# Kernel optimization log

Measured on AMD Instinct MI355X. Metric: run time of the kernel, lower is better.

Reference implementation:

```python
import jax, jax.numpy as jnp
import numpy as np

N_IN, N_LAT, LEN_T, N_SHIFT = 128, 21, 51, 50
N_HID, BATCH = 4, 2048


def identity_init(n_rows, n_cols):
    A = np.zeros((n_rows, n_cols), np.float32)
    if n_rows >= n_cols:
        k = n_rows - n_cols + 1
        for c in range(n_cols):
            A[c:c + k, c] = 1.0 / k
    else:
        k = n_cols - n_rows + 1
        for r in range(n_rows):
            A[r, r:r + k] = 1.0 / k
    return jnp.asarray(A)


def setup_inputs() -> dict:
    key = jax.random.key(0)
    ks = jax.random.split(key, 8)
    s = 0.05
    return {
        'inputs': jax.random.normal(ks[0], (BATCH, LEN_T, N_IN), dtype=jnp.float32),
        'enc_W': jax.random.normal(ks[1], (N_HID, N_IN, N_IN), dtype=jnp.float32) * s,
        'enc_b': jnp.zeros((N_HID, N_IN), jnp.float32),
        'enc_Wout': jax.random.normal(ks[2], (N_IN, N_IN), dtype=jnp.float32) * s,
        'enc_bout': jnp.zeros((N_IN,), jnp.float32),
        'dec_W': jax.random.normal(ks[3], (N_HID, N_IN, N_IN), dtype=jnp.float32) * s,
        'dec_b': jnp.zeros((N_HID, N_IN), jnp.float32),
        'dec_Wout': jax.random.normal(ks[4], (N_IN, N_IN), dtype=jnp.float32) * s,
        'dec_bout': jnp.zeros((N_IN,), jnp.float32),
        'W_enc_inner': identity_init(N_IN, N_LAT),
        'L': jnp.eye(N_LAT, dtype=jnp.float32),
        'W_dec_inner': identity_init(N_LAT, N_IN),
    }


def res_block(x, Ws, bs, Wout, bout):
    # DenseResBlock: ReLU hidden dense stack + linear output + identity skip
    h = x
    for i in range(Ws.shape[0]):
        h = jax.nn.relu(h @ Ws[i] + bs[i])
    return h @ Wout + bout + x


def reference(inputs, enc_W, enc_b, enc_Wout, enc_bout,
              dec_W, dec_b, dec_Wout, dec_bout,
              W_enc_inner, L, W_dec_inner):
    B = inputs.shape[0]
    len_pred = LEN_T - N_SHIFT  # = 1

    # ---- autoencoder branch (all timesteps flattened into rows) ----
    auto_in = inputs.reshape(-1, N_IN)                       # [B*T, n_in]
    part_enc = res_block(auto_in, enc_W, enc_b, enc_Wout, enc_bout)
    full_enc = part_enc @ W_enc_inner                        # [B*T, n_lat]
    part_dec = full_enc @ W_dec_inner                        # [B*T, n_in]
    autoencoder_output = res_block(part_dec, dec_W, dec_b, dec_Wout, dec_bout)
    autoencoder_output = autoencoder_output.reshape(B, LEN_T, N_IN)
    outer_auto_output = res_block(part_enc, dec_W, dec_b, dec_Wout, dec_bout)
    outer_auto_output = outer_auto_output.reshape(B, LEN_T, N_IN)

    # ---- prediction branch: recurrent application of Koopman operator L ----
    pred_in = inputs[:, :len_pred, :].reshape(-1, N_IN)      # [B*len_pred, n_in]
    cur = res_block(pred_in, enc_W, enc_b, enc_Wout, enc_bout) @ W_enc_inner

    def step(cur_enc, _):
        adv = cur_enc @ L                                    # [B*len_pred, n_lat]
        dec = res_block(adv @ W_dec_inner, dec_W, dec_b, dec_Wout, dec_bout)
        return adv, dec

    _, preds = jax.lax.scan(step, cur, None, length=N_SHIFT)  # [S, B*lp, n_in]
    preds = preds.reshape(N_SHIFT, B, len_pred, N_IN)
    predictions = preds.transpose(1, 0, 2, 3).reshape(B, N_SHIFT * len_pred, N_IN)

    return autoencoder_output, outer_auto_output, predictions
```

## Files before the change

### kernel.cpp

```cpp
#include <hip/hip_runtime.h>
#include <stdint.h>


typedef _Float16 h8 __attribute__((ext_vector_type(8)));
typedef _Float16 h4 __attribute__((ext_vector_type(4)));
typedef float    f4 __attribute__((ext_vector_type(4)));

#define ROWS_AUTO 104448
#define NT64      1632
#define NUNITS    2432

#define WT_ENCW      0
#define WT_ENCWOUT   (4*16384)
#define WT_DECW      (5*16384)
#define WT_DECWOUT   (9*16384)
#define WT_COMB      (10*16384)

#define MFULL_OFF_B 0x60000
#define ACH_OFF_B   0x200000
#define PE_OFF_B    0x220000
#define PET0_OFF_B  0x1C00000
#define CTRL_OFF_B  0x1D00000

#define H0 0
#define H1 16384
#define H2 32768
#define H3 49152
#define LDSE (49152 + 2560 + 16)
#define LDSD (65536 + 2560 + 16)

#define hsw(rl, c) ((rl)*256 + ((((c)) ^ ((rl) & 7)) << 4))

#define PIN(B) asm volatile("" : "+v"(B[0]), "+v"(B[1]), "+v"(B[2]), "+v"(B[3]), \
                                 "+v"(B[4]), "+v"(B[5]), "+v"(B[6]), "+v"(B[7]))

__device__ __forceinline__ f4 mfma16(h8 a, h8 b, f4 c) {
  return __builtin_amdgcn_mfma_f32_16x16x32_f16(a, b, c, 0, 0, 0);
}
__device__ __forceinline__ h8 cvt8(f4 a, f4 b) {
  h8 r;
  r[0]=(_Float16)a[0]; r[1]=(_Float16)a[1]; r[2]=(_Float16)a[2]; r[3]=(_Float16)a[3];
  r[4]=(_Float16)b[0]; r[5]=(_Float16)b[1]; r[6]=(_Float16)b[2]; r[7]=(_Float16)b[3];
  return r;
}
__device__ __forceinline__ void loadW(h8 B[8], const _Float16* gW, int nbase, int r15, int hi) {
#pragma unroll
  for (int nt = 0; nt < 2; ++nt)
#pragma unroll
    for (int ks = 0; ks < 4; ++ks)
      B[nt*4+ks] = *(const h8*)(gW + (size_t)(nbase + nt*16 + r15)*128 + ks*32 + hi*8);
}

__device__ __forceinline__ void mmF4s(const char* sm, int hb, const h8 B[8],
                                      f4 acc[4][2], int r15, int hi) {
#pragma unroll
  for (int rt = 0; rt < 4; ++rt) { acc[rt][0] = (f4){0,0,0,0}; acc[rt][1] = (f4){0,0,0,0}; }
#pragma unroll
  for (int ks = 0; ks < 4; ++ks) {
    int c = ks*4 + hi;
    h8 a[4];
#pragma unroll
    for (int rt = 0; rt < 4; ++rt) a[rt] = *(const h8*)(sm + hb + hsw(rt*16 + r15, c));
#pragma unroll
    for (int rt = 0; rt < 4; ++rt) {
      acc[rt][0] = mfma16(B[ks],   a[rt], acc[rt][0]);
      acc[rt][1] = mfma16(B[4+ks], a[rt], acc[rt][1]);
    }
  }
}

__device__ __forceinline__ void hw4s(char* sm, int hb, int wbase, const f4 acc[4][2],
                                     const float* bl, int bo, int r15, int hi) {
  f4 bb0 = *(const f4*)(bl + bo + wbase + hi*4);
  f4 bb1 = *(const f4*)(bl + bo + wbase + 16 + hi*4);
  int bo2 = (hi & 1) * 8;
#pragma unroll
  for (int nt = 0; nt < 2; ++nt) {
    int c = ((wbase + nt*16) >> 3) + (hi >> 1);
    f4 bb = nt ? bb1 : bb0;
#pragma unroll
    for (int rt = 0; rt < 4; ++rt) {
      int row = rt*16 + r15;
      h4 p;
#pragma unroll
      for (int d = 0; d < 4; ++d) p[d] = (_Float16)fmaxf(acc[rt][nt][d] + bb[d], 0.f);
      *(h4*)(sm + hb + row*256 + ((c ^ (row & 7)) << 4) + bo2) = p;
    }
  }
}
__device__ __forceinline__ void hw4r(char* sm, int hb, int wbase, const f4 acc[4][2],
                                     int r15, int hi) {
  int bo2 = (hi & 1) * 8;
#pragma unroll
  for (int nt = 0; nt < 2; ++nt) {
    int c = ((wbase + nt*16) >> 3) + (hi >> 1);
#pragma unroll
    for (int rt = 0; rt < 4; ++rt) {
      int row = rt*16 + r15;
      h4 p;
#pragma unroll
      for (int d = 0; d < 4; ++d) p[d] = (_Float16)acc[rt][nt][d];
      *(h4*)(sm + hb + row*256 + ((c ^ (row & 7)) << 4) + bo2) = p;
    }
  }
}

__device__ __forceinline__ void epi_direct(const char* sm, int hskip, int wbase,
                                           const f4 acc[4][2], const float* bl,
                                           float* dst, int rstride, int r15, int hi) {
  f4 bb0 = *(const f4*)(bl + 512 + wbase + hi*4);
  f4 bb1 = *(const f4*)(bl + 512 + wbase + 16 + hi*4);
  int bo2 = (hi & 1) * 8;
#pragma unroll
  for (int nt = 0; nt < 2; ++nt) {
    int c = ((wbase + nt*16) >> 3) + (hi >> 1);
    int n0 = wbase + nt*16 + hi*4;
    f4 bb = nt ? bb1 : bb0;
#pragma unroll
    for (int rt = 0; rt < 4; ++rt) {
      int row = rt*16 + r15;
      h4 sk = *(const h4*)(sm + hskip + row*256 + ((c ^ (row & 7)) << 4) + bo2);
      f4 v;
#pragma unroll
      for (int d = 0; d < 4; ++d) v[d] = acc[rt][nt][d] + bb[d] + (float)sk[d];
      *(f4*)(dst + (size_t)row*rstride + n0) = v;
    }
  }
}

#define LAYD(HIN, HOUT, BW, BO) do {                                 \
    mmF4s(sm, HIN, BW, acc, r15, hi);                                \
    hw4s(sm, HOUT, wbase, acc, bl, BO, r15, hi);                     \
    __syncthreads();                                                 \
  } while (0)

#define TICKET(CTR, LIM, VAR)                                        \
    __syncthreads();                                                 \
    if (tid == 0) *tk = __hip_atomic_fetch_add(&(CTR), 1,            \
                          __ATOMIC_RELAXED, __HIP_MEMORY_SCOPE_AGENT); \
    __syncthreads();                                                 \
    int VAR = *tk;                                                   \
    if (VAR >= (LIM)) break;


__global__ __launch_bounds__(512) void k_prep(
    const float* __restrict__ encW, const float* __restrict__ encWout,
    const float* __restrict__ decW, const float* __restrict__ decWout,
    const float* __restrict__ L,
    _Float16* __restrict__ wt, float* __restrict__ ach) {
  __shared__ float chA[441], chB[441];
  int m = blockIdx.y, tid = threadIdx.x;
  if (m == 10) {
    if (blockIdx.x != 0) return;
    if (tid < 441) chA[tid] = L[tid];
    __syncthreads();
    for (int s = 0; s < 50; ++s) {
      if (tid < 441) ach[s*441 + tid] = chA[tid];
      if (s == 49) break;
      if (tid < 441) {
        int i = tid / 21, j = tid % 21; float a = 0.f;
        for (int k = 0; k < 21; ++k) a += chA[i*21 + k] * L[k*21 + j];
        chB[tid] = a;
      }
      __syncthreads();
      if (tid < 441) chA[tid] = chB[tid];
      __syncthreads();
    }
    return;
  }
  int idx = blockIdx.x*512 + tid;
  if (idx >= 16384) return;
  const float* src; _Float16* dst;
  if (m < 4)       { src = encW + m*16384;     dst = wt + WT_ENCW + m*16384; }
  else if (m == 4) { src = encWout;            dst = wt + WT_ENCWOUT; }
  else if (m < 9)  { src = decW + (m-5)*16384; dst = wt + WT_DECW + (m-5)*16384; }
  else             { src = decWout;            dst = wt + WT_DECWOUT; }
  int n = idx >> 7, k = idx & 127;
  dst[idx] = (_Float16)src[k*128 + n];
}

__global__ __launch_bounds__(512) void k_aux(
    const float* __restrict__ ach, const float* __restrict__ wencI,
    const float* __restrict__ wdecI,
    _Float16* __restrict__ mfull, _Float16* __restrict__ wt) {
  __shared__ float T1[2688];
  __shared__ float sa[441];
  int s = blockIdx.x, t = threadIdx.x;
  if (s < 50) {
    if (t < 441) sa[t] = ach[s*441 + t];
    __syncthreads();
    for (int idx = t; idx < 2688; idx += 512) {
      int k = idx / 21, j = idx % 21;
      float a = 0.f;
      for (int u = 0; u < 21; ++u) a += wencI[k*21 + u] * sa[u*21 + j];
      T1[idx] = a;
    }
  } else {
    for (int idx = t; idx < 2688; idx += 512) T1[idx] = wencI[idx];
  }
  __syncthreads();
  _Float16* dst = (s < 50) ? (mfull + (size_t)s*16384) : (wt + WT_COMB);
  for (int idx = t; idx < 16384; idx += 512) {
    int n = idx >> 7, k = idx & 127;
    float a = 0.f;
    for (int j = 0; j < 21; ++j) a += T1[k*21 + j] * wdecI[j*128 + n];
    dst[idx] = (_Float16)a;
  }
}


__global__ __launch_bounds__(256, 2) void k_enc(
    const float* __restrict__ x, const _Float16* __restrict__ wt,
    const float* __restrict__ enc_b, const float* __restrict__ enc_bout,
    _Float16* __restrict__ pe_ws, _Float16* __restrict__ pet0,
    int* __restrict__ ctrl) {
  __shared__ char sm[LDSE];
  float* bl = (float*)(sm + 49152);
  int* tk = (int*)(sm + 49152 + 2560);
  int tid = threadIdx.x, lane = tid & 63;
  int r15 = lane & 15, hi = lane >> 4;
  int wbase = (tid >> 6) * 32;
  h8 B0[8], B1[8], B2[8], B3[8], B4[8];
  loadW(B0, wt + WT_ENCW,           wbase, r15, hi);
  loadW(B1, wt + WT_ENCW + 16384,   wbase, r15, hi);
  loadW(B2, wt + WT_ENCW + 2*16384, wbase, r15, hi);
  loadW(B3, wt + WT_ENCW + 3*16384, wbase, r15, hi);
  loadW(B4, wt + WT_ENCWOUT,        wbase, r15, hi);
  PIN(B0); PIN(B1); PIN(B2); PIN(B3); PIN(B4);
  bl[tid] = enc_b[tid]; bl[256 + tid] = enc_b[256 + tid];
  if (tid < 128) bl[512 + tid] = enc_bout[tid];
  f4 acc[4][2];

  for (;;) {
    TICKET(ctrl[0], NT64, t);
    size_t rb = (size_t)t * 64;
#pragma unroll
    for (int i = 0; i < 4; ++i) {
      int idx = i*256 + tid, rl = idx >> 4, c = idx & 15;
      const float* s = x + (rb + rl)*128 + c*8;
      f4 v0 = *(const f4*)s, v1 = *(const f4*)(s + 4);
      *(h8*)(sm + H0 + hsw(rl, c)) = cvt8(v0, v1);
    }
    __syncthreads();
    LAYD(H0, H1, B0, 0); LAYD(H1, H2, B1, 128);
    LAYD(H2, H1, B2, 256); LAYD(H1, H2, B3, 384);
    mmF4s(sm, H2, B4, acc, r15, hi);
    {
      f4 bb0 = *(const f4*)(bl + 512 + wbase + hi*4);
      f4 bb1 = *(const f4*)(bl + 512 + wbase + 16 + hi*4);
      int bo2 = (hi & 1) * 8;
#pragma unroll
      for (int nt = 0; nt < 2; ++nt) {
        int c = ((wbase + nt*16) >> 3) + (hi >> 1);
        f4 bb = nt ? bb1 : bb0;
#pragma unroll
        for (int rt = 0; rt < 4; ++rt) {
          int row = rt*16 + r15;
          int soff = H0 + row*256 + ((c ^ (row & 7)) << 4) + bo2;
          h4 sk = *(const h4*)(sm + soff);
          h4 p;
#pragma unroll
          for (int d = 0; d < 4; ++d) p[d] = (_Float16)(acc[rt][nt][d] + bb[d] + (float)sk[d]);
          *(h4*)(sm + soff) = p;
        }
      }
    }
    __syncthreads();
    {
      char* g = (char*)(pe_ws) + (size_t)t*16384;
#pragma unroll
      for (int i = 0; i < 4; ++i) {
        int idx = i*256 + tid, off = idx*16;
        f4 v = *(const f4*)(sm + H0 + off);
        *(f4*)(g + off) = v;
        int rl = idx >> 4, slot = idx & 15;
        size_t rg = rb + (size_t)rl;
        if (rg % 51u == 0u) {
          int c = slot ^ (rl & 7);
          *(f4*)((char*)pet0 + (rg/51u)*256 + c*16) = v;
        }
      }
    }
  }
}


__global__ __launch_bounds__(256, 2) void k_decpred(
    const _Float16* __restrict__ wt, const _Float16* __restrict__ pe_ws,
    const _Float16* __restrict__ pet0, const _Float16* __restrict__ mfull,
    const float* __restrict__ dec_b, const float* __restrict__ dec_bout,
    float* __restrict__ out1, float* __restrict__ out2, float* __restrict__ out3,
    int* __restrict__ ctrl) {
  __shared__ char sm[LDSD];
  float* bl = (float*)(sm + 65536);
  int* tk = (int*)(sm + 65536 + 2560);
  int tid = threadIdx.x, lane = tid & 63;
  int r15 = lane & 15, hi = lane >> 4;
  int wbase = (tid >> 6) * 32;
  h8 B0[8], B1[8], B2[8], B3[8], B4[8];
  loadW(B0, wt + WT_DECW,           wbase, r15, hi);
  loadW(B1, wt + WT_DECW + 16384,   wbase, r15, hi);
  loadW(B2, wt + WT_DECW + 2*16384, wbase, r15, hi);
  loadW(B3, wt + WT_DECW + 3*16384, wbase, r15, hi);
  loadW(B4, wt + WT_DECWOUT,        wbase, r15, hi);
  PIN(B0); PIN(B1); PIN(B2); PIN(B3); PIN(B4);
  bl[tid] = dec_b[tid]; bl[256 + tid] = dec_b[256 + tid];
  if (tid < 128) bl[512 + tid] = dec_bout[tid];
  f4 acc[4][2];

  for (;;) {
    TICKET(ctrl[1], NUNITS, u);
    if (u < NT64) {
      const char* src = (const char*)pe_ws + (size_t)u*16384;
#pragma unroll
      for (int i = 0; i < 4; ++i) {
        int off = (i*256 + tid)*16;
        *(f4*)(sm + H0 + off) = *(const f4*)(src + off);
      }
      __syncthreads();
      LAYD(H0, H1, B0, 0); LAYD(H1, H2, B1, 128);
      LAYD(H2, H1, B2, 256); LAYD(H1, H2, B3, 384);
      mmF4s(sm, H2, B4, acc, r15, hi);
      epi_direct(sm, H0, wbase, acc, bl,
                 out2 + (size_t)u*64*128, 128, r15, hi);
      {
        h8 Bc[8];
        loadW(Bc, wt + WT_COMB, wbase, r15, hi);
        mmF4s(sm, H0, Bc, acc, r15, hi);
      }
      hw4r(sm, H3, wbase, acc, r15, hi);
      __syncthreads();
      LAYD(H3, H0, B0, 0); LAYD(H0, H1, B1, 128);
      LAYD(H1, H0, B2, 256); LAYD(H0, H1, B3, 384);
      mmF4s(sm, H1, B4, acc, r15, hi);
      epi_direct(sm, H3, wbase, acc, bl,
                 out1 + (size_t)u*64*128, 128, r15, hi);
    } else {
      int p = u - NT64, rtile = p / 25, chunk = p % 25;
#pragma unroll
      for (int i = 0; i < 4; ++i) {
        int idx = i*256 + tid, rl = idx >> 4, c = idx & 15;
        f4 v = *(const f4*)((const char*)pet0 + (size_t)(rtile*64 + rl)*256 + c*16);
        *(f4*)(sm + H0 + hsw(rl, c)) = v;
      }
      __syncthreads();
      for (int s = chunk*2; s < chunk*2 + 2; ++s) {
        {
          h8 Bm[8];
          loadW(Bm, mfull + (size_t)s*16384, wbase, r15, hi);
          mmF4s(sm, H0, Bm, acc, r15, hi);
        }
        hw4r(sm, H1, wbase, acc, r15, hi);
        __syncthreads();
        LAYD(H1, H2, B0, 0); LAYD(H2, H3, B1, 128);
        LAYD(H3, H2, B2, 256); LAYD(H2, H3, B3, 384);
        mmF4s(sm, H3, B4, acc, r15, hi);
        epi_direct(sm, H1, wbase, acc, bl,
                   out3 + ((size_t)rtile*64*50 + s)*128, 50*128, r15, hi);
        __syncthreads();
      }
    }
  }
}


extern "C" void kernel_launch(void* const* d_in, const int* in_sizes, int n_in,
                              void* d_out, int out_size, void* d_ws, size_t ws_size,
                              hipStream_t stream) {
  const float* x        = (const float*)d_in[0];
  const float* encW     = (const float*)d_in[1];
  const float* enc_b    = (const float*)d_in[2];
  const float* encWout  = (const float*)d_in[3];
  const float* enc_bout = (const float*)d_in[4];
  const float* decW     = (const float*)d_in[5];
  const float* dec_b    = (const float*)d_in[6];
  const float* decWout  = (const float*)d_in[7];
  const float* dec_bout = (const float*)d_in[8];
  const float* wencI    = (const float*)d_in[9];
  const float* L        = (const float*)d_in[10];
  const float* wdecI    = (const float*)d_in[11];

  char* ws = (char*)d_ws;
  _Float16* wt    = (_Float16*)ws;
  _Float16* mfull = (_Float16*)(ws + MFULL_OFF_B);
  float*    ach   = (float*)(ws + ACH_OFF_B);
  _Float16* pe_ws = (_Float16*)(ws + PE_OFF_B);
  _Float16* pet0  = (_Float16*)(ws + PET0_OFF_B);
  int*      ctrl  = (int*)(ws + CTRL_OFF_B);

  float* out1 = (float*)d_out;
  float* out2 = out1 + (size_t)ROWS_AUTO*128;
  float* out3 = out2 + (size_t)ROWS_AUTO*128;

  hipMemsetAsync(ctrl, 0, sizeof(int)*2, stream);
  hipLaunchKernelGGL(k_prep, dim3(32, 11), dim3(512), 0, stream,
                     encW, encWout, decW, decWout, L, wt, ach);
  hipLaunchKernelGGL(k_aux, dim3(51), dim3(512), 0, stream,
                     ach, wencI, wdecI, mfull, wt);
  hipLaunchKernelGGL(k_enc, dim3(512), dim3(256), 0, stream,
                     x, wt, enc_b, enc_bout, pe_ws, pet0, ctrl);
  hipLaunchKernelGGL(k_decpred, dim3(512), dim3(256), 0, stream,
                     wt, pe_ws, pet0, mfull, dec_b, dec_bout, out1, out2, out3, ctrl);
}
```

Measured before the change: 208.4 us.

## Use 512-thread blocks processing two independent 64-row chains interleaved per barrier

Blocks grow from 256 to 512 threads. Eight waves split each 64-row tile into two 32-row halves, and each block now processes two independent work streams at once: two encoder tiles, the two decoder chains per tile, or two prediction steps. Their layers are interleaved so each barrier covers twice the MFMA work and the two chains overlap. This costs a much larger LDS footprint per block (about 100-117KB) and 512 threads each pinning five weight fragments in registers, which may limit occupancy to one block per CU.

```diff
diff --git a/kernel.cpp b/kernel.cpp
--- a/kernel.cpp
+++ b/kernel.cpp
@@ -8,6 +8,7 @@
 
 #define ROWS_AUTO 104448
 #define NT64      1632
+#define NPAIR     816
 #define NUNITS    2432
 
 #define WT_ENCW      0
@@ -22,12 +23,21 @@
 #define PET0_OFF_B  0x1C00000
 #define CTRL_OFF_B  0x1D00000
 
-#define H0 0
-#define H1 16384
-#define H2 32768
-#define H3 49152
-#define LDSE (49152 + 2560 + 16)
-#define LDSD (65536 + 2560 + 16)
+#define PA 0
+#define PB 16384
+#define UA 32768
+#define VA 49152
+#define UB 65536
+#define VB 81920
+#define LDSE (98304 + 2560 + 16)
+#define PP 0
+#define QQ 16384
+#define UU 32768
+#define VV 49152
+#define XX 65536
+#define YY 81920
+#define ZZ 98304
+#define LDSD (114688 + 2560 + 16)
 
 #define hsw(rl, c) ((rl)*256 + ((((c)) ^ ((rl) & 7)) << 4))
 
@@ -51,26 +61,24 @@
       B[nt*4+ks] = *(const h8*)(gW + (size_t)(nbase + nt*16 + r15)*128 + ks*32 + hi*8);
 }
 
-__device__ __forceinline__ void mmF4s(const char* sm, int hb, const h8 B[8],
-                                      f4 acc[4][2], int r15, int hi) {
-#pragma unroll
-  for (int rt = 0; rt < 4; ++rt) { acc[rt][0] = (f4){0,0,0,0}; acc[rt][1] = (f4){0,0,0,0}; }
+__device__ __forceinline__ void mm32(const char* sm, int hb, const h8 B[8],
+                                     f4 acc[2][2], int rb, int r15, int hi) {
+#pragma unroll
+  for (int rt = 0; rt < 2; ++rt) { acc[rt][0] = (f4){0,0,0,0}; acc[rt][1] = (f4){0,0,0,0}; }
 #pragma unroll
   for (int ks = 0; ks < 4; ++ks) {
     int c = ks*4 + hi;
-    h8 a[4];
-#pragma unroll
-    for (int rt = 0; rt < 4; ++rt) a[rt] = *(const h8*)(sm + hb + hsw(rt*16 + r15, c));
-#pragma unroll
-    for (int rt = 0; rt < 4; ++rt) {
-      acc[rt][0] = mfma16(B[ks],   a[rt], acc[rt][0]);
-      acc[rt][1] = mfma16(B[4+ks], a[rt], acc[rt][1]);
-    }
-  }
-}
-
-__device__ __forceinline__ void hw4s(char* sm, int hb, int wbase, const f4 acc[4][2],
-                                     const float* bl, int bo, int r15, int hi) {
+    h8 a0 = *(const h8*)(sm + hb + hsw(rb + r15, c));
+    h8 a1 = *(const h8*)(sm + hb + hsw(rb + 16 + r15, c));
+    acc[0][0] = mfma16(B[ks],   a0, acc[0][0]);
+    acc[0][1] = mfma16(B[4+ks], a0, acc[0][1]);
+    acc[1][0] = mfma16(B[ks],   a1, acc[1][0]);
+    acc[1][1] = mfma16(B[4+ks], a1, acc[1][1]);
+  }
+}
+
+__device__ __forceinline__ void hw32s(char* sm, int hb, int rb, int wbase, const f4 acc[2][2],
+                                      const float* bl, int bo, int r15, int hi) {
   f4 bb0 = *(const f4*)(bl + bo + wbase + hi*4);
   f4 bb1 = *(const f4*)(bl + bo + wbase + 16 + hi*4);
   int bo2 = (hi & 1) * 8;
@@ -79,8 +87,8 @@
     int c = ((wbase + nt*16) >> 3) + (hi >> 1);
     f4 bb = nt ? bb1 : bb0;
 #pragma unroll
-    for (int rt = 0; rt < 4; ++rt) {
-      int row = rt*16 + r15;
+    for (int rt = 0; rt < 2; ++rt) {
+      int row = rb + rt*16 + r15;
       h4 p;
 #pragma unroll
       for (int d = 0; d < 4; ++d) p[d] = (_Float16)fmaxf(acc[rt][nt][d] + bb[d], 0.f);
@@ -88,15 +96,15 @@
     }
   }
 }
-__device__ __forceinline__ void hw4r(char* sm, int hb, int wbase, const f4 acc[4][2],
-                                     int r15, int hi) {
+__device__ __forceinline__ void hw32r(char* sm, int hb, int rb, int wbase, const f4 acc[2][2],
+                                      int r15, int hi) {
   int bo2 = (hi & 1) * 8;
 #pragma unroll
   for (int nt = 0; nt < 2; ++nt) {
     int c = ((wbase + nt*16) >> 3) + (hi >> 1);
 #pragma unroll
-    for (int rt = 0; rt < 4; ++rt) {
-      int row = rt*16 + r15;
+    for (int rt = 0; rt < 2; ++rt) {
+      int row = rb + rt*16 + r15;
       h4 p;
 #pragma unroll
       for (int d = 0; d < 4; ++d) p[d] = (_Float16)acc[rt][nt][d];
@@ -105,9 +113,9 @@
   }
 }
 
-__device__ __forceinline__ void epi_direct(const char* sm, int hskip, int wbase,
-                                           const f4 acc[4][2], const float* bl,
-                                           float* dst, int rstride, int r15, int hi) {
+__device__ __forceinline__ void epi32(const char* sm, int hskip, int rb, int wbase,
+                                      const f4 acc[2][2], const float* bl,
+                                      float* dst, int rstride, int r15, int hi) {
   f4 bb0 = *(const f4*)(bl + 512 + wbase + hi*4);
   f4 bb1 = *(const f4*)(bl + 512 + wbase + 16 + hi*4);
   int bo2 = (hi & 1) * 8;
@@ -117,8 +125,8 @@
     int n0 = wbase + nt*16 + hi*4;
     f4 bb = nt ? bb1 : bb0;
 #pragma unroll
-    for (int rt = 0; rt < 4; ++rt) {
-      int row = rt*16 + r15;
+    for (int rt = 0; rt < 2; ++rt) {
+      int row = rb + rt*16 + r15;
       h4 sk = *(const h4*)(sm + hskip + row*256 + ((c ^ (row & 7)) << 4) + bo2);
       f4 v;
 #pragma unroll
@@ -127,12 +135,6 @@
     }
   }
 }
-
-#define LAYD(HIN, HOUT, BW, BO) do {                                 \
-    mmF4s(sm, HIN, BW, acc, r15, hi);                                \
-    hw4s(sm, HOUT, wbase, acc, bl, BO, r15, hi);                     \
-    __syncthreads();                                                 \
-  } while (0)
 
 #define TICKET(CTR, LIM, VAR)                                        \
     __syncthreads();                                                 \
@@ -209,17 +211,17 @@
 }
 
 
-__global__ __launch_bounds__(256, 2) void k_enc(
+__global__ __launch_bounds__(512, 2) void k_enc(
     const float* __restrict__ x, const _Float16* __restrict__ wt,
     const float* __restrict__ enc_b, const float* __restrict__ enc_bout,
     _Float16* __restrict__ pe_ws, _Float16* __restrict__ pet0,
     int* __restrict__ ctrl) {
   __shared__ char sm[LDSE];
-  float* bl = (float*)(sm + 49152);
-  int* tk = (int*)(sm + 49152 + 2560);
-  int tid = threadIdx.x, lane = tid & 63;
+  float* bl = (float*)(sm + 98304);
+  int* tk = (int*)(sm + 98304 + 2560);
+  int tid = threadIdx.x, lane = tid & 63, w = tid >> 6;
   int r15 = lane & 15, hi = lane >> 4;
-  int wbase = (tid >> 6) * 32;
+  int rb = (w >> 2) * 32, wbase = (w & 3) * 32;
   h8 B0[8], B1[8], B2[8], B3[8], B4[8];
   loadW(B0, wt + WT_ENCW,           wbase, r15, hi);
   loadW(B1, wt + WT_ENCW + 16384,   wbase, r15, hi);
@@ -227,24 +229,37 @@
   loadW(B3, wt + WT_ENCW + 3*16384, wbase, r15, hi);
   loadW(B4, wt + WT_ENCWOUT,        wbase, r15, hi);
   PIN(B0); PIN(B1); PIN(B2); PIN(B3); PIN(B4);
-  bl[tid] = enc_b[tid]; bl[256 + tid] = enc_b[256 + tid];
+  if (tid < 512) bl[tid] = enc_b[tid];
   if (tid < 128) bl[512 + tid] = enc_bout[tid];
-  f4 acc[4][2];
+  f4 aA[2][2], aB[2][2];
 
   for (;;) {
-    TICKET(ctrl[0], NT64, t);
-    size_t rb = (size_t)t * 64;
-#pragma unroll
-    for (int i = 0; i < 4; ++i) {
-      int idx = i*256 + tid, rl = idx >> 4, c = idx & 15;
-      const float* s = x + (rb + rl)*128 + c*8;
-      f4 v0 = *(const f4*)s, v1 = *(const f4*)(s + 4);
-      *(h8*)(sm + H0 + hsw(rl, c)) = cvt8(v0, v1);
-    }
-    __syncthreads();
-    LAYD(H0, H1, B0, 0); LAYD(H1, H2, B1, 128);
-    LAYD(H2, H1, B2, 256); LAYD(H1, H2, B3, 384);
-    mmF4s(sm, H2, B4, acc, r15, hi);
+    TICKET(ctrl[0], NPAIR, v);
+    int tA = v*2, tB = v*2 + 1;
+    size_t rbA = (size_t)tA * 64, rbB = (size_t)tB * 64;
+#pragma unroll
+    for (int i = 0; i < 2; ++i) {
+      int idx = i*512 + tid, rl = idx >> 4, c = idx & 15;
+      const float* sA = x + (rbA + rl)*128 + c*8;
+      const float* sB = x + (rbB + rl)*128 + c*8;
+      *(h8*)(sm + PA + hsw(rl, c)) = cvt8(*(const f4*)sA, *(const f4*)(sA + 4));
+      *(h8*)(sm + PB + hsw(rl, c)) = cvt8(*(const f4*)sB, *(const f4*)(sB + 4));
+    }
+    __syncthreads();
+    mm32(sm, PA, B0, aA, rb, r15, hi); hw32s(sm, UA, rb, wbase, aA, bl, 0, r15, hi);
+    mm32(sm, PB, B0, aB, rb, r15, hi); hw32s(sm, UB, rb, wbase, aB, bl, 0, r15, hi);
+    __syncthreads();
+    mm32(sm, UA, B1, aA, rb, r15, hi); hw32s(sm, VA, rb, wbase, aA, bl, 128, r15, hi);
+    mm32(sm, UB, B1, aB, rb, r15, hi); hw32s(sm, VB, rb, wbase, aB, bl, 128, r15, hi);
+    __syncthreads();
+    mm32(sm, VA, B2, aA, rb, r15, hi); hw32s(sm, UA, rb, wbase, aA, bl, 256, r15, hi);
+    mm32(sm, VB, B2, aB, rb, r15, hi); hw32s(sm, UB, rb, wbase, aB, bl, 256, r15, hi);
+    __syncthreads();
+    mm32(sm, UA, B3, aA, rb, r15, hi); hw32s(sm, VA, rb, wbase, aA, bl, 384, r15, hi);
+    mm32(sm, UB, B3, aB, rb, r15, hi); hw32s(sm, VB, rb, wbase, aB, bl, 384, r15, hi);
+    __syncthreads();
+    mm32(sm, VA, B4, aA, rb, r15, hi);
+    mm32(sm, VB, B4, aB, rb, r15, hi);
     {
       f4 bb0 = *(const f4*)(bl + 512 + wbase + hi*4);
       f4 bb1 = *(const f4*)(bl + 512 + wbase + 16 + hi*4);
@@ -254,49 +269,57 @@
         int c = ((wbase + nt*16) >> 3) + (hi >> 1);
         f4 bb = nt ? bb1 : bb0;
 #pragma unroll
-        for (int rt = 0; rt < 4; ++rt) {
-          int row = rt*16 + r15;
-          int soff = H0 + row*256 + ((c ^ (row & 7)) << 4) + bo2;
-          h4 sk = *(const h4*)(sm + soff);
-          h4 p;
-#pragma unroll
-          for (int d = 0; d < 4; ++d) p[d] = (_Float16)(acc[rt][nt][d] + bb[d] + (float)sk[d]);
-          *(h4*)(sm + soff) = p;
+        for (int rt = 0; rt < 2; ++rt) {
+          int row = rb + rt*16 + r15;
+          int so = row*256 + ((c ^ (row & 7)) << 4) + bo2;
+          h4 skA = *(const h4*)(sm + PA + so);
+          h4 skB = *(const h4*)(sm + PB + so);
+          h4 pA_, pB_;
+#pragma unroll
+          for (int d = 0; d < 4; ++d) {
+            pA_[d] = (_Float16)(aA[rt][nt][d] + bb[d] + (float)skA[d]);
+            pB_[d] = (_Float16)(aB[rt][nt][d] + bb[d] + (float)skB[d]);
+          }
+          *(h4*)(sm + PA + so) = pA_;
+          *(h4*)(sm + PB + so) = pB_;
         }
       }
     }
     __syncthreads();
     {
-      char* g = (char*)(pe_ws) + (size_t)t*16384;
-#pragma unroll
-      for (int i = 0; i < 4; ++i) {
-        int idx = i*256 + tid, off = idx*16;
-        f4 v = *(const f4*)(sm + H0 + off);
-        *(f4*)(g + off) = v;
+      char* gA = (char*)pe_ws + (size_t)tA*16384;
+      char* gB = (char*)pe_ws + (size_t)tB*16384;
+#pragma unroll
+      for (int i = 0; i < 2; ++i) {
+        int idx = i*512 + tid, off = idx*16;
+        f4 vA = *(const f4*)(sm + PA + off);
+        f4 vB = *(const f4*)(sm + PB + off);
+        *(f4*)(gA + off) = vA;
+        *(f4*)(gB + off) = vB;
         int rl = idx >> 4, slot = idx & 15;
-        size_t rg = rb + (size_t)rl;
-        if (rg % 51u == 0u) {
-          int c = slot ^ (rl & 7);
-          *(f4*)((char*)pet0 + (rg/51u)*256 + c*16) = v;
-        }
-      }
-    }
-  }
-}
-
-
-__global__ __launch_bounds__(256, 2) void k_decpred(
+        int c = slot ^ (rl & 7);
+        size_t rgA = rbA + (size_t)rl;
+        size_t rgB = rbB + (size_t)rl;
+        if (rgA % 51u == 0u) *(f4*)((char*)pet0 + (rgA/51u)*256 + c*16) = vA;
+        if (rgB % 51u == 0u) *(f4*)((char*)pet0 + (rgB/51u)*256 + c*16) = vB;
+      }
+    }
+  }
+}
+
+
+__global__ __launch_bounds__(512, 2) void k_decpred(
     const _Float16* __restrict__ wt, const _Float16* __restrict__ pe_ws,
     const _Float16* __restrict__ pet0, const _Float16* __restrict__ mfull,
     const float* __restrict__ dec_b, const float* __restrict__ dec_bout,
     float* __restrict__ out1, float* __restrict__ out2, float* __restrict__ out3,
     int* __restrict__ ctrl) {
   __shared__ char sm[LDSD];
-  float* bl = (float*)(sm + 65536);
-  int* tk = (int*)(sm + 65536 + 2560);
-  int tid = threadIdx.x, lane = tid & 63;
+  float* bl = (float*)(sm + 114688);
+  int* tk = (int*)(sm + 114688 + 2560);
+  int tid = threadIdx.x, lane = tid & 63, w = tid >> 6;
   int r15 = lane & 15, hi = lane >> 4;
-  int wbase = (tid >> 6) * 32;
+  int rb = (w >> 2) * 32, wbase = (w & 3) * 32;
   h8 B0[8], B1[8], B2[8], B3[8], B4[8];
   loadW(B0, wt + WT_DECW,           wbase, r15, hi);
   loadW(B1, wt + WT_DECW + 16384,   wbase, r15, hi);
@@ -304,61 +327,82 @@
   loadW(B3, wt + WT_DECW + 3*16384, wbase, r15, hi);
   loadW(B4, wt + WT_DECWOUT,        wbase, r15, hi);
   PIN(B0); PIN(B1); PIN(B2); PIN(B3); PIN(B4);
-  bl[tid] = dec_b[tid]; bl[256 + tid] = dec_b[256 + tid];
+  if (tid < 512) bl[tid] = dec_b[tid];
   if (tid < 128) bl[512 + tid] = dec_bout[tid];
-  f4 acc[4][2];
+  f4 aB_[2][2], aA_[2][2];
 
   for (;;) {
     TICKET(ctrl[1], NUNITS, u);
     if (u < NT64) {
       const char* src = (const char*)pe_ws + (size_t)u*16384;
 #pragma unroll
-      for (int i = 0; i < 4; ++i) {
-        int off = (i*256 + tid)*16;
-        *(f4*)(sm + H0 + off) = *(const f4*)(src + off);
-      }
-      __syncthreads();
-      LAYD(H0, H1, B0, 0); LAYD(H1, H2, B1, 128);
-      LAYD(H2, H1, B2, 256); LAYD(H1, H2, B3, 384);
-      mmF4s(sm, H2, B4, acc, r15, hi);
-      epi_direct(sm, H0, wbase, acc, bl,
-                 out2 + (size_t)u*64*128, 128, r15, hi);
+      for (int i = 0; i < 2; ++i) {
+        int off = (i*512 + tid)*16;
+        *(f4*)(sm + PP + off) = *(const f4*)(src + off);
+      }
+      __syncthreads();
       {
         h8 Bc[8];
         loadW(Bc, wt + WT_COMB, wbase, r15, hi);
-        mmF4s(sm, H0, Bc, acc, r15, hi);
-      }
-      hw4r(sm, H3, wbase, acc, r15, hi);
-      __syncthreads();
-      LAYD(H3, H0, B0, 0); LAYD(H0, H1, B1, 128);
-      LAYD(H1, H0, B2, 256); LAYD(H0, H1, B3, 384);
-      mmF4s(sm, H1, B4, acc, r15, hi);
-      epi_direct(sm, H3, wbase, acc, bl,
-                 out1 + (size_t)u*64*128, 128, r15, hi);
+        mm32(sm, PP, Bc, aA_, rb, r15, hi);
+      }
+      hw32r(sm, QQ, rb, wbase, aA_, r15, hi);
+      mm32(sm, PP, B0, aB_, rb, r15, hi); hw32s(sm, UU, rb, wbase, aB_, bl, 0, r15, hi);
+      __syncthreads();
+      mm32(sm, UU, B1, aB_, rb, r15, hi); hw32s(sm, VV, rb, wbase, aB_, bl, 128, r15, hi);
+      mm32(sm, QQ, B0, aA_, rb, r15, hi); hw32s(sm, XX, rb, wbase, aA_, bl, 0,   r15, hi);
+      __syncthreads();
+      mm32(sm, VV, B2, aB_, rb, r15, hi); hw32s(sm, UU, rb, wbase, aB_, bl, 256, r15, hi);
+      mm32(sm, XX, B1, aA_, rb, r15, hi); hw32s(sm, YY, rb, wbase, aA_, bl, 128, r15, hi);
+      __syncthreads();
+      mm32(sm, UU, B3, aB_, rb, r15, hi); hw32s(sm, VV, rb, wbase, aB_, bl, 384, r15, hi);
+      mm32(sm, YY, B2, aA_, rb, r15, hi); hw32s(sm, XX, rb, wbase, aA_, bl, 256, r15, hi);
+      __syncthreads();
+      mm32(sm, VV, B4, aB_, rb, r15, hi);
+      epi32(sm, PP, rb, wbase, aB_, bl, out2 + (size_t)u*64*128, 128, r15, hi);
+      mm32(sm, XX, B3, aA_, rb, r15, hi); hw32s(sm, YY, rb, wbase, aA_, bl, 384, r15, hi);
+      __syncthreads();
+      mm32(sm, YY, B4, aA_, rb, r15, hi);
+      epi32(sm, QQ, rb, wbase, aA_, bl, out1 + (size_t)u*64*128, 128, r15, hi);
     } else {
-      int p = u - NT64, rtile = p / 25, chunk = p % 25;
-#pragma unroll
-      for (int i = 0; i < 4; ++i) {
-        int idx = i*256 + tid, rl = idx >> 4, c = idx & 15;
+      int p = u - NT64, rtile = p / 25, s0 = (p % 25) * 2;
+#pragma unroll
+      for (int i = 0; i < 2; ++i) {
+        int idx = i*512 + tid, rl = idx >> 4, c = idx & 15;
         f4 v = *(const f4*)((const char*)pet0 + (size_t)(rtile*64 + rl)*256 + c*16);
-        *(f4*)(sm + H0 + hsw(rl, c)) = v;
-      }
-      __syncthreads();
-      for (int s = chunk*2; s < chunk*2 + 2; ++s) {
-        {
-          h8 Bm[8];
-          loadW(Bm, mfull + (size_t)s*16384, wbase, r15, hi);
-          mmF4s(sm, H0, Bm, acc, r15, hi);
-        }
-        hw4r(sm, H1, wbase, acc, r15, hi);
-        __syncthreads();
-        LAYD(H1, H2, B0, 0); LAYD(H2, H3, B1, 128);
-        LAYD(H3, H2, B2, 256); LAYD(H2, H3, B3, 384);
-        mmF4s(sm, H3, B4, acc, r15, hi);
-        epi_direct(sm, H1, wbase, acc, bl,
-                   out3 + ((size_t)rtile*64*50 + s)*128, 50*128, r15, hi);
-        __syncthreads();
-      }
+        *(f4*)(sm + PP + hsw(rl, c)) = v;
+      }
+      __syncthreads();
+      {
+        h8 Bm[8];
+        loadW(Bm, mfull + (size_t)s0*16384, wbase, r15, hi);
+        mm32(sm, PP, Bm, aB_, rb, r15, hi);
+      }
+      hw32r(sm, QQ, rb, wbase, aB_, r15, hi);
+      {
+        h8 Bm[8];
+        loadW(Bm, mfull + (size_t)(s0+1)*16384, wbase, r15, hi);
+        mm32(sm, PP, Bm, aA_, rb, r15, hi);
+      }
+      hw32r(sm, XX, rb, wbase, aA_, r15, hi);
+      __syncthreads();
+      mm32(sm, QQ, B0, aB_, rb, r15, hi); hw32s(sm, UU, rb, wbase, aB_, bl, 0, r15, hi);
+      mm32(sm, XX, B0, aA_, rb, r15, hi); hw32s(sm, YY, rb, wbase, aA_, bl, 0, r15, hi);
+      __syncthreads();
+      mm32(sm, UU, B1, aB_, rb, r15, hi); hw32s(sm, VV, rb, wbase, aB_, bl, 128, r15, hi);
+      mm32(sm, YY, B1, aA_, rb, r15, hi); hw32s(sm, ZZ, rb, wbase, aA_, bl, 128, r15, hi);
+      __syncthreads();
+      mm32(sm, VV, B2, aB_, rb, r15, hi); hw32s(sm, UU, rb, wbase, aB_, bl, 256, r15, hi);
+      mm32(sm, ZZ, B2, aA_, rb, r15, hi); hw32s(sm, YY, rb, wbase, aA_, bl, 256, r15, hi);
+      __syncthreads();
+      mm32(sm, UU, B3, aB_, rb, r15, hi); hw32s(sm, VV, rb, wbase, aB_, bl, 384, r15, hi);
+      mm32(sm, YY, B3, aA_, rb, r15, hi); hw32s(sm, ZZ, rb, wbase, aA_, bl, 384, r15, hi);
+      __syncthreads();
+      float* d3 = out3 + (size_t)rtile*64*50*128;
+      mm32(sm, VV, B4, aB_, rb, r15, hi);
+      epi32(sm, QQ, rb, wbase, aB_, bl, d3 + (size_t)s0*128, 50*128, r15, hi);
+      mm32(sm, ZZ, B4, aA_, rb, r15, hi);
+      epi32(sm, XX, rb, wbase, aA_, bl, d3 + (size_t)(s0+1)*128, 50*128, r15, hi);
     }
   }
 }
@@ -397,8 +441,8 @@
                      encW, encWout, decW, decWout, L, wt, ach);
   hipLaunchKernelGGL(k_aux, dim3(51), dim3(512), 0, stream,
                      ach, wencI, wdecI, mfull, wt);
-  hipLaunchKernelGGL(k_enc, dim3(512), dim3(256), 0, stream,
+  hipLaunchKernelGGL(k_enc, dim3(256), dim3(512), 0, stream,
                      x, wt, enc_b, enc_bout, pe_ws, pet0, ctrl);
-  hipLaunchKernelGGL(k_decpred, dim3(512), dim3(256), 0, stream,
+  hipLaunchKernelGGL(k_decpred, dim3(256), dim3(512), 0, stream,
                      wt, pe_ws, pet0, mfull, dec_b, dec_bout, out1, out2, out3, ctrl);
 }
```

After: 233.4 us. +12.0%, slower.
